# Optimization experiments

Hardware: AMD Instinct MI355X
Metric: run time of the kernel (lower is better)

## Reference

```python
import jax, jax.numpy as jnp
import numpy as np

L = 8192        # sequence length
C = 256         # channels
S = 64          # state_dim
SAMPLE_RATE = 16000.0


def setup_inputs() -> dict:
    key = jax.random.key(0)
    kx, kc = jax.random.split(key)
    x = jax.random.normal(kx, (L, C), dtype=jnp.float32)
    # Params exactly as flax init: A = -(1..S), stored as log(-A), broadcast over channels
    lognegA = jnp.broadcast_to(jnp.log(jnp.arange(1, S + 1, dtype=jnp.float32)), (C, S))
    lognegA = jnp.array(lognegA)  # materialize
    B = jnp.ones((C, S), dtype=jnp.float32)
    # nn.initializers.normal() default stddev = 0.01
    Cp = 0.01 * jax.random.normal(kc, (C, S), dtype=jnp.float32)
    return {"x": x, "lognegA": lognegA, "B": B, "Cp": Cp}


def reference(x, lognegA, B, Cp):
    length = x.shape[0]
    dt = 1.0 / SAMPLE_RATE
    A = -jnp.exp(lognegA)                                  # (C, S), all negative
    # discretized input matrix: Bd = (exp(A*dt) - 1) * B / A
    Bd = (jnp.exp(A * dt) - 1.0) * B / A                    # (C, S)
    # Ak[l, c, s] = exp(l * A[c, s] * dt)
    Ak = jnp.exp(jnp.einsum('l,cs->lcs', jnp.arange(length, dtype=x.dtype), A * dt))
    # K[l, c] = sum_s Cp[c,s] * Ak[l,c,s] * Bd[c,s]
    K = jnp.einsum('cs,lcs,cs->lc', Cp, Ak, Bd)             # (L, C)
    # per-channel full convolution, truncated to first L samples (causal conv)
    y = jax.vmap(jnp.convolve, in_axes=1, out_axes=1)(x, K)[:length]
    return y
```

## Files before the change

kernel.cpp:

```cpp
#include <hip/hip_runtime.h>
#include <math.h>

#define LSEQ 8192
#define CCH  256
#define SDIM 64
#define PCHUNK 256
#define CLEN (LSEQ / PCHUNK)
#define DT (1.0 / 16000.0)

__global__ void s4d_params(const float* __restrict__ lognegA,
                           const float* __restrict__ B,
                           const float* __restrict__ Cp,
                           float* __restrict__ rt,
                           float* __restrict__ wt,
                           float* __restrict__ rPt) {
    int idx = blockIdx.x * blockDim.x + threadIdx.x;
    if (idx >= CCH * SDIM) return;
    int c = idx / SDIM;
    int s = idx % SDIM;
    double A   = -exp((double)lognegA[idx]);
    double adt = A * DT;
    double r   = exp(adt);
    double Bd  = expm1(adt) * (double)B[idx] / A;
    double w   = (double)Cp[idx] * Bd;
    rt [s * CCH + c] = (float)r;
    wt [s * CCH + c] = (float)w;
    rPt[s * CCH + c] = (float)exp(adt * (double)CLEN);
}

__global__ __launch_bounds__(256, 1) void s4d_local(const float* __restrict__ x,
                                                    const float* __restrict__ rt,
                                                    float* __restrict__ st) {
    int wave = blockIdx.x * (blockDim.x >> 6) + (threadIdx.x >> 6);
    int lane = threadIdx.x & 63;
    int cb = wave >> 8;
    int p  = wave & (PCHUNK - 1);
    int c  = cb * 64 + lane;

    float rr[SDIM], h[SDIM];
#pragma unroll
    for (int s = 0; s < SDIM; ++s) {
        rr[s] = rt[s * CCH + c];
        h[s]  = 0.0f;
    }
    const float* xp = x + (size_t)(p * CLEN) * CCH + c;
#pragma unroll 2
    for (int i = 0; i < CLEN; ++i) {
        float xv = xp[(size_t)i * CCH];
#pragma unroll
        for (int s = 0; s < SDIM; ++s)
            h[s] = fmaf(rr[s], h[s], xv);
    }
#pragma unroll
    for (int s = 0; s < SDIM; ++s)
        st[(size_t)(s * PCHUNK + p) * CCH + c] = h[s];
}

__global__ void s4d_scan(const float* __restrict__ rPt,
                         float* __restrict__ st) {
    int wave = blockIdx.x * (blockDim.x >> 6) + (threadIdx.x >> 6);
    int lane = threadIdx.x & 63;
    int s  = wave >> 2;
    int cb = wave & 3;
    int c  = cb * 64 + lane;
    float rp = rPt[s * CCH + c];
    float state = 0.0f;
    for (int p = 0; p < PCHUNK; ++p) {
        size_t idx = (size_t)(s * PCHUNK + p) * CCH + c;
        float e = st[idx];
        st[idx] = state;
        state = fmaf(rp, state, e);
    }
}

__global__ __launch_bounds__(256, 1) void s4d_final(const float* __restrict__ x,
                                                    const float* __restrict__ rt,
                                                    const float* __restrict__ wt,
                                                    const float* __restrict__ st,
                                                    float* __restrict__ y) {
    int wave = blockIdx.x * (blockDim.x >> 6) + (threadIdx.x >> 6);
    int lane = threadIdx.x & 63;
    int cb = wave >> 8;
    int p  = wave & (PCHUNK - 1);
    int c  = cb * 64 + lane;

    float rr[SDIM], ww[SDIM], h[SDIM];
#pragma unroll
    for (int s = 0; s < SDIM; ++s) {
        rr[s] = rt[s * CCH + c];
        ww[s] = wt[s * CCH + c];
        h[s]  = st[(size_t)(s * PCHUNK + p) * CCH + c];
    }
    const float* xp = x + (size_t)(p * CLEN) * CCH + c;
    float*       yp = y + (size_t)(p * CLEN) * CCH + c;
#pragma unroll 2
    for (int i = 0; i < CLEN; ++i) {
        float xv = xp[(size_t)i * CCH];
        float acc0 = 0.0f, acc1 = 0.0f;
#pragma unroll
        for (int s = 0; s < SDIM; s += 2) {
            h[s]     = fmaf(rr[s],     h[s],     xv);
            acc0     = fmaf(ww[s],     h[s],     acc0);
            h[s + 1] = fmaf(rr[s + 1], h[s + 1], xv);
            acc1     = fmaf(ww[s + 1], h[s + 1], acc1);
        }
        yp[(size_t)i * CCH] = acc0 + acc1;
    }
}

extern "C" void kernel_launch(void* const* d_in, const int* in_sizes, int n_in,
                              void* d_out, int out_size, void* d_ws, size_t ws_size,
                              hipStream_t stream) {
    const float* x       = (const float*)d_in[0];
    const float* lognegA = (const float*)d_in[1];
    const float* B       = (const float*)d_in[2];
    const float* Cp      = (const float*)d_in[3];
    float* out = (float*)d_out;

    float* ws  = (float*)d_ws;
    float* rt  = ws;
    float* wt  = rt  + CCH * SDIM;
    float* rPt = wt  + CCH * SDIM;
    float* st  = rPt + CCH * SDIM;

    s4d_params<<<(CCH * SDIM + 255) / 256, 256, 0, stream>>>(lognegA, B, Cp, rt, wt, rPt);
    s4d_local<<<(4 * PCHUNK) / 4, 256, 0, stream>>>(x, rt, st);
    s4d_scan<<<(SDIM * 4) / 4, 256, 0, stream>>>(rPt, st);
    s4d_final<<<(4 * PCHUNK) / 4, 256, 0, stream>>>(x, rt, wt, st, out);
}
```

Measured before the change: 101.9 us.

## Fuse params, local scan, chunk scan and final pass into one persistent kernel

Replaces the four kernel launches with a single kernel of 256 blocks that sync through software grid barriers built on atomics, plus a memset to reset the barrier counters. Parameters are recomputed inline in float32 with a polynomial expm1 instead of a separate double-precision parameter kernel. The x chunk is held in registers across both passes, and the chunk-state scan is split over 4 waves combined through shared memory, which gives the scan more parallelism. The aim is to remove launch gaps and extra memory traffic, at the cost of spin-wait barriers, a dependence on all 256 blocks being resident at once, and slightly lower parameter precision.

```diff
diff --git a/kernel.cpp b/kernel.cpp
--- a/kernel.cpp
+++ b/kernel.cpp
@@ -5,106 +5,134 @@
 #define CCH  256
 #define SDIM 64
 #define PCHUNK 256
-#define CLEN (LSEQ / PCHUNK)
-#define DT (1.0 / 16000.0)
+#define CLEN 32
+#define NBLK 256
 
-__global__ void s4d_params(const float* __restrict__ lognegA,
-                           const float* __restrict__ B,
-                           const float* __restrict__ Cp,
-                           float* __restrict__ rt,
-                           float* __restrict__ wt,
-                           float* __restrict__ rPt) {
-    int idx = blockIdx.x * blockDim.x + threadIdx.x;
-    if (idx >= CCH * SDIM) return;
-    int c = idx / SDIM;
-    int s = idx % SDIM;
-    double A   = -exp((double)lognegA[idx]);
-    double adt = A * DT;
-    double r   = exp(adt);
-    double Bd  = expm1(adt) * (double)B[idx] / A;
-    double w   = (double)Cp[idx] * Bd;
-    rt [s * CCH + c] = (float)r;
-    wt [s * CCH + c] = (float)w;
-    rPt[s * CCH + c] = (float)exp(adt * (double)CLEN);
+__device__ __forceinline__ void gbar(unsigned* ctr) {
+    __syncthreads();
+    if (threadIdx.x == 0) {
+        __threadfence();
+        __hip_atomic_fetch_add(ctr, 1u, __ATOMIC_RELEASE, __HIP_MEMORY_SCOPE_AGENT);
+        while (__hip_atomic_load(ctr, __ATOMIC_ACQUIRE, __HIP_MEMORY_SCOPE_AGENT) < (unsigned)NBLK) {
+            __builtin_amdgcn_s_sleep(1);
+        }
+        __threadfence();
+    }
+    __syncthreads();
 }
 
-__global__ __launch_bounds__(256, 1) void s4d_local(const float* __restrict__ x,
-                                                    const float* __restrict__ rt,
-                                                    float* __restrict__ st) {
-    int wave = blockIdx.x * (blockDim.x >> 6) + (threadIdx.x >> 6);
-    int lane = threadIdx.x & 63;
-    int cb = wave >> 8;
-    int p  = wave & (PCHUNK - 1);
-    int c  = cb * 64 + lane;
+__device__ __forceinline__ float expm1_small(float z) {
+    return z * (1.0f + z * (0.5f + z * (0.16666667f + z * 0.041666668f)));
+}
 
-    float rr[SDIM], h[SDIM];
+__global__ __launch_bounds__(256, 1) void s4d_one(
+    const float* __restrict__ x,
+    const float* __restrict__ lognegA,
+    const float* __restrict__ Bm,
+    const float* __restrict__ Cp,
+    float* __restrict__ y,
+    float* __restrict__ st,
+    unsigned* __restrict__ bars)
+{
+    const int lane = threadIdx.x & 63;
+    const int wl   = threadIdx.x >> 6;
+    const int b    = blockIdx.x;
+    const int c    = wl * 64 + lane;
+    const float dt = 6.25e-05f;
+
+    float xv[CLEN];
+    {
+        const float* xp = x + (size_t)(b * CLEN) * CCH + c;
 #pragma unroll
-    for (int s = 0; s < SDIM; ++s) {
-        rr[s] = rt[s * CCH + c];
-        h[s]  = 0.0f;
+        for (int i = 0; i < CLEN; ++i) xv[i] = xp[(size_t)i * CCH];
     }
-    const float* xp = x + (size_t)(p * CLEN) * CCH + c;
-#pragma unroll 2
-    for (int i = 0; i < CLEN; ++i) {
-        float xv = xp[(size_t)i * CCH];
+
+    {
+        float rr[SDIM], h[SDIM];
+        const float* lnaP = lognegA + c * SDIM;
+#pragma unroll
+        for (int s = 0; s < SDIM; ++s) {
+            float A   = -expf(lnaP[s]);
+            rr[s] = 1.0f + expm1_small(A * dt);
+            h[s]  = 0.0f;
+        }
+#pragma unroll
+        for (int i = 0; i < CLEN; ++i) {
+            float xi = xv[i];
+#pragma unroll
+            for (int s = 0; s < SDIM; ++s)
+                h[s] = fmaf(rr[s], h[s], xi);
+        }
 #pragma unroll
         for (int s = 0; s < SDIM; ++s)
-            h[s] = fmaf(rr[s], h[s], xv);
+            st[(size_t)(s * PCHUNK + b) * CCH + c] = h[s];
     }
+    gbar(bars + 0);
+
+    {
+        const int s2 = b >> 2;
+        const int c2 = (b & 3) * 64 + lane;
+        float A    = -expf(lognegA[c2 * SDIM + s2]);
+        float adt  = A * dt;
+        float rP   = expf(adt * 32.0f);
+        float rP64 = expf(adt * 2048.0f);
+
+        float e[64];
+        size_t base = ((size_t)s2 * PCHUNK + wl * 64) * CCH + c2;
 #pragma unroll
-    for (int s = 0; s < SDIM; ++s)
-        st[(size_t)(s * PCHUNK + p) * CCH + c] = h[s];
-}
+        for (int j = 0; j < 64; ++j) e[j] = st[base + (size_t)j * CCH];
 
-__global__ void s4d_scan(const float* __restrict__ rPt,
-                         float* __restrict__ st) {
-    int wave = blockIdx.x * (blockDim.x >> 6) + (threadIdx.x >> 6);
-    int lane = threadIdx.x & 63;
-    int s  = wave >> 2;
-    int cb = wave & 3;
-    int c  = cb * 64 + lane;
-    float rp = rPt[s * CCH + c];
-    float state = 0.0f;
-    for (int p = 0; p < PCHUNK; ++p) {
-        size_t idx = (size_t)(s * PCHUNK + p) * CCH + c;
-        float e = st[idx];
-        st[idx] = state;
-        state = fmaf(rp, state, e);
+        float agg = 0.0f;
+#pragma unroll
+        for (int j = 0; j < 64; ++j) agg = fmaf(rP, agg, e[j]);
+
+        __shared__ float aggs[4][64];
+        aggs[wl][lane] = agg;
+        __syncthreads();
+
+        float sin = 0.0f;
+#pragma unroll
+        for (int v = 0; v < 3; ++v)
+            if (v < wl) sin = fmaf(rP64, sin, aggs[v][lane]);
+
+#pragma unroll
+        for (int j = 0; j < 64; ++j) {
+            st[base + (size_t)j * CCH] = sin;
+            sin = fmaf(rP, sin, e[j]);
+        }
     }
-}
+    gbar(bars + 1);
 
-__global__ __launch_bounds__(256, 1) void s4d_final(const float* __restrict__ x,
-                                                    const float* __restrict__ rt,
-                                                    const float* __restrict__ wt,
-                                                    const float* __restrict__ st,
-                                                    float* __restrict__ y) {
-    int wave = blockIdx.x * (blockDim.x >> 6) + (threadIdx.x >> 6);
-    int lane = threadIdx.x & 63;
-    int cb = wave >> 8;
-    int p  = wave & (PCHUNK - 1);
-    int c  = cb * 64 + lane;
+    {
+        float rr[SDIM], ww[SDIM], h[SDIM];
+        const float* lnaP = lognegA + c * SDIM;
+        const float* BP   = Bm + c * SDIM;
+        const float* CpP  = Cp + c * SDIM;
+#pragma unroll
+        for (int s = 0; s < SDIM; ++s) {
+            float A   = -expf(lnaP[s]);
+            float em  = expm1_small(A * dt);
+            rr[s] = 1.0f + em;
+            ww[s] = CpP[s] * (em * BP[s] / A);
+        }
+#pragma unroll
+        for (int s = 0; s < SDIM; ++s)
+            h[s] = st[(size_t)(s * PCHUNK + b) * CCH + c];
 
-    float rr[SDIM], ww[SDIM], h[SDIM];
+        float* yp = y + (size_t)(b * CLEN) * CCH + c;
 #pragma unroll
-    for (int s = 0; s < SDIM; ++s) {
-        rr[s] = rt[s * CCH + c];
-        ww[s] = wt[s * CCH + c];
-        h[s]  = st[(size_t)(s * PCHUNK + p) * CCH + c];
-    }
-    const float* xp = x + (size_t)(p * CLEN) * CCH + c;
-    float*       yp = y + (size_t)(p * CLEN) * CCH + c;
-#pragma unroll 2
-    for (int i = 0; i < CLEN; ++i) {
-        float xv = xp[(size_t)i * CCH];
-        float acc0 = 0.0f, acc1 = 0.0f;
+        for (int i = 0; i < CLEN; ++i) {
+            float xi = xv[i];
+            float a0 = 0.0f, a1 = 0.0f;
 #pragma unroll
-        for (int s = 0; s < SDIM; s += 2) {
-            h[s]     = fmaf(rr[s],     h[s],     xv);
-            acc0     = fmaf(ww[s],     h[s],     acc0);
-            h[s + 1] = fmaf(rr[s + 1], h[s + 1], xv);
-            acc1     = fmaf(ww[s + 1], h[s + 1], acc1);
+            for (int s = 0; s < SDIM; s += 2) {
+                h[s]     = fmaf(rr[s],     h[s],     xi);
+                a0       = fmaf(ww[s],     h[s],     a0);
+                h[s + 1] = fmaf(rr[s + 1], h[s + 1], xi);
+                a1       = fmaf(ww[s + 1], h[s + 1], a1);
+            }
+            yp[(size_t)i * CCH] = a0 + a1;
         }
-        yp[(size_t)i * CCH] = acc0 + acc1;
     }
 }
 
@@ -113,18 +141,13 @@
                               hipStream_t stream) {
     const float* x       = (const float*)d_in[0];
     const float* lognegA = (const float*)d_in[1];
-    const float* B       = (const float*)d_in[2];
+    const float* Bm      = (const float*)d_in[2];
     const float* Cp      = (const float*)d_in[3];
     float* out = (float*)d_out;
 
-    float* ws  = (float*)d_ws;
-    float* rt  = ws;
-    float* wt  = rt  + CCH * SDIM;
-    float* rPt = wt  + CCH * SDIM;
-    float* st  = rPt + CCH * SDIM;
+    unsigned* bars = (unsigned*)d_ws;
+    float*    st   = (float*)d_ws + 64;
 
-    s4d_params<<<(CCH * SDIM + 255) / 256, 256, 0, stream>>>(lognegA, B, Cp, rt, wt, rPt);
-    s4d_local<<<(4 * PCHUNK) / 4, 256, 0, stream>>>(x, rt, st);
-    s4d_scan<<<(SDIM * 4) / 4, 256, 0, stream>>>(rPt, st);
-    s4d_final<<<(4 * PCHUNK) / 4, 256, 0, stream>>>(x, rt, wt, st, out);
+    hipMemsetAsync(bars, 0, 256, stream);
+    s4d_one<<<dim3(NBLK), dim3(256), 0, stream>>>(x, lognegA, Bm, Cp, out, st, bars);
 }
```

Result: slower. 159.4 us (+56.5%).
